# Kernel tuning notes

Hardware: AMD Instinct MI355X
Metric: run time of the kernel (lower is better)

Reference implementation:

```python
import jax, jax.numpy as jnp
import numpy as np

H = 512   # hidden_size
V = 128   # vec_size / output_size
L = 8192  # sequence length


def _gru_cell(x, h, Wih, Whh, bih, bhh):
    # torch GRU cell: gates ordered (r, z, n)
    gx = x @ Wih.T + bih            # [3H]
    gh = h @ Whh.T + bhh            # [3H]
    xr, xz, xn = jnp.split(gx, 3)
    hr, hz, hn = jnp.split(gh, 3)
    r = jax.nn.sigmoid(xr + hr)
    z = jax.nn.sigmoid(xz + hz)
    n = jnp.tanh(xn + r * hn)
    return (1.0 - z) * n + z * h


def _run_gru2(xs, h0, h1, p0, p1):
    """2-layer GRU over xs [L, in]; returns ((h0_f, h1_f), top-layer outputs [L, H])."""
    def step(carry, x):
        c0, c1 = carry
        c0 = _gru_cell(x, c0, *p0)
        c1 = _gru_cell(c0, c1, *p1)
        return (c0, c1), c1
    return jax.lax.scan(step, (h0, h1), xs)


def setup_inputs() -> dict:
    key = jax.random.key(0)
    ks = jax.random.split(key, 24)
    b = 1.0 / np.sqrt(H)  # torch default uniform init bound
    u = lambda k, shape: jax.random.uniform(k, shape, jnp.float32, -b, b)
    inp = {
        "src": jax.random.normal(ks[0], (L, V), jnp.float32),
        "trg": jax.random.uniform(ks[1], (L, V), jnp.float32),
        # encoder GRU (input V -> hidden H, 2 layers)
        "enc_Wih0": u(ks[2], (3 * H, V)),  "enc_Whh0": u(ks[3], (3 * H, H)),
        "enc_bih0": u(ks[4], (3 * H,)),    "enc_bhh0": u(ks[5], (3 * H,)),
        "enc_Wih1": u(ks[6], (3 * H, H)),  "enc_Whh1": u(ks[7], (3 * H, H)),
        "enc_bih1": u(ks[8], (3 * H,)),    "enc_bhh1": u(ks[9], (3 * H,)),
        # decoder GRU (input V -> hidden H, 2 layers)
        "dec_Wih0": u(ks[10], (3 * H, V)), "dec_Whh0": u(ks[11], (3 * H, H)),
        "dec_bih0": u(ks[12], (3 * H,)),   "dec_bhh0": u(ks[13], (3 * H,)),
        "dec_Wih1": u(ks[14], (3 * H, H)), "dec_Whh1": u(ks[15], (3 * H, H)),
        "dec_bih1": u(ks[16], (3 * H,)),   "dec_bhh1": u(ks[17], (3 * H,)),
        # output projection
        "Wout": u(ks[18], (V, H)), "bout": u(ks[19], (V,)),
    }
    return inp


def reference(src, trg,
              enc_Wih0, enc_Whh0, enc_bih0, enc_bhh0,
              enc_Wih1, enc_Whh1, enc_bih1, enc_bhh1,
              dec_Wih0, dec_Whh0, dec_bih0, dec_bhh0,
              dec_Wih1, dec_Whh1, dec_bih1, dec_bhh1,
              Wout, bout):
    z = jnp.zeros((H,), src.dtype)
    # Encoder: run 2-layer GRU over src, keep final per-layer states
    (h0, h1), _ = _run_gru2(
        src, z, z,
        (enc_Wih0, enc_Whh0, enc_bih0, enc_bhh0),
        (enc_Wih1, enc_Whh1, enc_bih1, enc_bhh1))
    # Decoder inputs under full teacher forcing: trg[0], trg[0], trg[1], ... trg[L-2]
    dec_in = jax.nn.relu(jnp.concatenate([trg[:1], trg[:-1]], axis=0))  # [L, V]
    _, ys = _run_gru2(
        dec_in, h0, h1,
        (dec_Wih0, dec_Whh0, dec_bih0, dec_bhh0),
        (dec_Wih1, dec_Whh1, dec_bih1, dec_bhh1))  # ys: [L, H] top-layer outputs
    outputs = jax.nn.sigmoid(ys @ Wout.T + bout)   # [L, V]
    return outputs
```

## Files before the change

kernel.cpp:

```cpp
#include <hip/hip_runtime.h>

#define Hh   512
#define Vv   128
#define LL   8192
#define G3   1536
#define NBK  256
#define NPAIR 1024

#define OFF_GX   0ull
#define OFF_YS   50331648ull
#define OFF_RECE 67108864ull
#define OFF_RECD (OFF_RECE + 16384ull)
#define OFF_WT   (OFF_RECD + 16384ull)

__device__ __forceinline__ float sigm(float x)  { return 1.f / (1.f + __expf(-x)); }
__device__ __forceinline__ float tanha(float x) { return 2.f / (1.f + __expf(-2.f * x)) - 1.f; }

__device__ __forceinline__ unsigned long long packpair(float v, int t) {
    return ((unsigned long long)(unsigned)t << 32) | (unsigned long long)__float_as_uint(v);
}
__device__ __forceinline__ int   pair_tag(unsigned long long p) { return (int)(p >> 32); }
__device__ __forceinline__ float pair_val(unsigned long long p) { return __uint_as_float((unsigned)p); }

__global__ __launch_bounds__(256) void gemm_gx(
    const float* __restrict__ X, const float* __restrict__ Wih,
    const float* __restrict__ bih, float* __restrict__ gxo, int shift_relu)
{
    __shared__ float xs[16][128];
    const int tid = threadIdx.x;
    const int m0  = blockIdx.x * 16;
    const int c   = blockIdx.y * 256 + tid;

    for (int i = tid; i < 16 * 128; i += 256) {
        const int r = i >> 7, k = i & 127;
        int srow = m0 + r;
        if (shift_relu) srow = (srow == 0) ? 0 : (srow - 1);
        float v = X[(size_t)srow * Vv + k];
        if (shift_relu) v = fmaxf(v, 0.f);
        xs[r][k] = v;
    }
    __syncthreads();

    const float4* wp = (const float4*)(Wih + (size_t)c * Vv);
    float4 wr[32];
#pragma unroll
    for (int q = 0; q < 32; ++q) wr[q] = wp[q];
    const float bb = bih[c];

    for (int m = 0; m < 16; ++m) {
        const float4* xp = (const float4*)xs[m];
        float acc = bb;
#pragma unroll
        for (int q = 0; q < 32; ++q) {
            const float4 x4 = xp[q];
            acc = fmaf(wr[q].x, x4.x, acc); acc = fmaf(wr[q].y, x4.y, acc);
            acc = fmaf(wr[q].z, x4.z, acc); acc = fmaf(wr[q].w, x4.w, acc);
        }
        gxo[(size_t)(m0 + m) * G3 + c] = acc;
    }
}

__global__ __launch_bounds__(64, 1) void seq2(
    const float* __restrict__ gx,
    const float* __restrict__ Whh0, const float* __restrict__ Wih1,
    const float* __restrict__ Whh1,
    const float* __restrict__ bhh0, const float* __restrict__ bih1,
    const float* __restrict__ bhh1,
    unsigned long long* __restrict__ rec,
    float* __restrict__ ys)
{
    const int bid  = blockIdx.x, lane = threadIdx.x;
    const int e0   = 2 * bid;

    int off[8];
#pragma unroll
    for (int j = 0; j < 8; ++j) off[j] = (e0 + lane + 64 * j) & 511;

    float w[18][8];
#pragma unroll
    for (int m = 0; m < 3; ++m) {
        const float* mat = (m == 0) ? Whh0 : (m == 1) ? Wih1 : Whh1;
#pragma unroll
        for (int g = 0; g < 3; ++g)
#pragma unroll
            for (int i = 0; i < 2; ++i) {
                const float* row = mat + (size_t)(g * Hh + e0 + i) * Hh;
#pragma unroll
                for (int j = 0; j < 8; ++j) w[m * 6 + g * 2 + i][j] = row[off[j]];
            }
    }

    float b_r = 0.f, b_z = 0.f, b_n1 = 0.f, b_n2 = 0.f;
    if (lane < 2) {
        const int e = e0 + lane;
        b_r = bhh0[e]; b_z = bhh0[Hh + e]; b_n1 = bhh0[2 * Hh + e];
    } else if (lane < 4) {
        const int e = e0 + (lane & 1);
        b_r  = bih1[e] + bhh1[e];
        b_z  = bih1[Hh + e] + bhh1[Hh + e];
        b_n1 = bih1[2 * Hh + e];
        b_n2 = bhh1[2 * Hh + e];
    }

    for (int tau = 0; tau <= LL; ++tau) {
        float xr = 0.f, xz = 0.f, xn = 0.f;
        if (lane < 2 && tau < LL) {
            const size_t gb = (size_t)tau * G3 + e0 + lane;
            xr = gx[gb]; xz = gx[gb + Hh]; xn = gx[gb + 2 * Hh];
        }

        const int need = tau - 1;
        const unsigned long long* rp = rec + (size_t)((tau - 1) & 1) * NPAIR;
        unsigned long long p0[8], p1[8];
        int ok;
        do {
#pragma unroll
            for (int j = 0; j < 8; ++j)
                p0[j] = __hip_atomic_load(rp + off[j],      __ATOMIC_RELAXED, __HIP_MEMORY_SCOPE_AGENT);
#pragma unroll
            for (int j = 0; j < 8; ++j)
                p1[j] = __hip_atomic_load(rp + Hh + off[j], __ATOMIC_RELAXED, __HIP_MEMORY_SCOPE_AGENT);
            ok = 1;
#pragma unroll
            for (int j = 0; j < 8; ++j)
                ok &= (pair_tag(p0[j]) >= need) & (pair_tag(p1[j]) >= need);
        } while (!__all(ok));

        float h0v[8], h1v[8];
#pragma unroll
        for (int j = 0; j < 8; ++j) { h0v[j] = pair_val(p0[j]); h1v[j] = pair_val(p1[j]); }

        float acc[18];
#pragma unroll
        for (int r = 0; r < 18; ++r) acc[r] = 0.f;
#pragma unroll
        for (int j = 0; j < 8; ++j) {
#pragma unroll
            for (int r = 0; r < 12; ++r) acc[r] = fmaf(w[r][j], h0v[j], acc[r]);
#pragma unroll
            for (int r = 12; r < 18; ++r) acc[r] = fmaf(w[r][j], h1v[j], acc[r]);
        }

        float sred[9];
#pragma unroll
        for (int k = 0; k < 9; ++k) {
            float a = acc[2 * k], c = acc[2 * k + 1];
            a += __shfl_xor(a, 1);
            c += __shfl_xor(c, 1);
            float m = (lane & 1) ? c : a;
            m += __shfl_xor(m, 2);  m += __shfl_xor(m, 4);
            m += __shfl_xor(m, 8);  m += __shfl_xor(m, 16);
            m += __shfl_xor(m, 32);
            sred[k] = m;
        }

        const float h1p = __shfl(h1v[0], lane & 1);

        unsigned long long* recw = rec + (size_t)(tau & 1) * NPAIR;
        if (lane < 2) {
            if (tau < LL) {
                const float rg = sigm(xr + sred[0] + b_r);
                const float zg = sigm(xz + sred[1] + b_z);
                const float ng = tanha(xn + rg * (sred[2] + b_n1));
                const float hnew = (1.f - zg) * ng + zg * h0v[0];
                __hip_atomic_store(recw + e0 + lane, packpair(hnew, tau),
                                   __ATOMIC_RELAXED, __HIP_MEMORY_SCOPE_AGENT);
            }
        } else if (lane < 4) {
            const int e = e0 + (lane & 1);
            float hnew;
            if (tau >= 1) {
                const float rg = sigm(sred[3] + sred[6] + b_r);
                const float zg = sigm(sred[4] + sred[7] + b_z);
                const float ng = tanha(sred[5] + b_n1 + rg * (sred[8] + b_n2));
                hnew = (1.f - zg) * ng + zg * h1p;
                if (ys) ys[(size_t)(tau - 1) * Hh + e] = hnew;
            } else {
                hnew = h1p;
            }
            __hip_atomic_store(recw + Hh + e, packpair(hnew, tau),
                               __ATOMIC_RELAXED, __HIP_MEMORY_SCOPE_AGENT);
        }
    }
}

__global__ __launch_bounds__(256) void transposeW(const float* __restrict__ W,
                                                  float* __restrict__ WT,
                                                  unsigned long long* __restrict__ encr)
{
    const int i = blockIdx.x * 256 + threadIdx.x;
    WT[(i & 511) * 128 + (i >> 9)] = W[i];
    if (i < NPAIR) {
        __hip_atomic_store(encr + NPAIR + i, packpair(0.f, -1),
                           __ATOMIC_RELAXED, __HIP_MEMORY_SCOPE_AGENT);
        __hip_atomic_store(encr + i, packpair(0.f, -2),
                           __ATOMIC_RELAXED, __HIP_MEMORY_SCOPE_AGENT);
    }
}

__global__ __launch_bounds__(256) void handoff(const unsigned long long* __restrict__ encr,
                                               unsigned long long* __restrict__ decr)
{
    const int p = blockIdx.x * 256 + threadIdx.x;
    const unsigned long long src = __hip_atomic_load(
        encr + (p < Hh ? NPAIR : 0) + p, __ATOMIC_RELAXED, __HIP_MEMORY_SCOPE_AGENT);
    __hip_atomic_store(decr + NPAIR + p, packpair(pair_val(src), -1),
                       __ATOMIC_RELAXED, __HIP_MEMORY_SCOPE_AGENT);
    __hip_atomic_store(decr + p, packpair(0.f, -2),
                       __ATOMIC_RELAXED, __HIP_MEMORY_SCOPE_AGENT);
}

__global__ __launch_bounds__(128) void out_proj(
    const float* __restrict__ ys, const float* __restrict__ WT,
    const float* __restrict__ bout, float* __restrict__ out)
{
    __shared__ float yss[16][512];
    const int tid = threadIdx.x;
    const int m0  = blockIdx.x * 16;

    for (int i = tid; i < 16 * 512; i += 128)
        yss[i >> 9][i & 511] = ys[(size_t)(m0 + (i >> 9)) * 512 + (i & 511)];
    __syncthreads();

    const int c = tid;
    float acc[16];
    const float b = bout[c];
#pragma unroll
    for (int m = 0; m < 16; ++m) acc[m] = b;

    for (int k4 = 0; k4 < 128; ++k4) {
        const float w0 = WT[(4 * k4 + 0) * 128 + c];
        const float w1 = WT[(4 * k4 + 1) * 128 + c];
        const float w2 = WT[(4 * k4 + 2) * 128 + c];
        const float w3 = WT[(4 * k4 + 3) * 128 + c];
#pragma unroll
        for (int m = 0; m < 16; ++m) {
            const float4 yv = *(const float4*)&yss[m][4 * k4];
            acc[m] = fmaf(w0, yv.x, fmaf(w1, yv.y, fmaf(w2, yv.z, fmaf(w3, yv.w, acc[m]))));
        }
    }
#pragma unroll
    for (int m = 0; m < 16; ++m)
        out[(size_t)(m0 + m) * 128 + c] = 1.f / (1.f + __expf(-acc[m]));
}

extern "C" void kernel_launch(void* const* d_in, const int* in_sizes, int n_in,
                              void* d_out, int out_size, void* d_ws, size_t ws_size,
                              hipStream_t stream)
{
    const float* src      = (const float*)d_in[0];
    const float* trg      = (const float*)d_in[1];
    const float* eWih0    = (const float*)d_in[2];
    const float* eWhh0    = (const float*)d_in[3];
    const float* ebih0    = (const float*)d_in[4];
    const float* ebhh0    = (const float*)d_in[5];
    const float* eWih1    = (const float*)d_in[6];
    const float* eWhh1    = (const float*)d_in[7];
    const float* ebih1    = (const float*)d_in[8];
    const float* ebhh1    = (const float*)d_in[9];
    const float* dWih0    = (const float*)d_in[10];
    const float* dWhh0    = (const float*)d_in[11];
    const float* dbih0    = (const float*)d_in[12];
    const float* dbhh0    = (const float*)d_in[13];
    const float* dWih1    = (const float*)d_in[14];
    const float* dWhh1    = (const float*)d_in[15];
    const float* dbih1    = (const float*)d_in[16];
    const float* dbhh1    = (const float*)d_in[17];
    const float* Wout     = (const float*)d_in[18];
    const float* bout     = (const float*)d_in[19];

    char* ws = (char*)d_ws;
    float*              gx   = (float*)(ws + OFF_GX);
    float*              ys   = (float*)(ws + OFF_YS);
    unsigned long long* recE = (unsigned long long*)(ws + OFF_RECE);
    unsigned long long* recD = (unsigned long long*)(ws + OFF_RECD);
    float*              WT   = (float*)(ws + OFF_WT);

    hipLaunchKernelGGL(transposeW, dim3(256), dim3(256), 0, stream, Wout, WT, recE);

    hipLaunchKernelGGL(gemm_gx, dim3(LL / 16, 6), dim3(256), 0, stream,
                       src, eWih0, ebih0, gx, 0);
    hipLaunchKernelGGL(seq2, dim3(NBK), dim3(64), 0, stream,
                       gx, eWhh0, eWih1, eWhh1, ebhh0, ebih1, ebhh1,
                       recE, (float*)nullptr);

    hipLaunchKernelGGL(handoff, dim3(4), dim3(256), 0, stream, recE, recD);
    hipLaunchKernelGGL(gemm_gx, dim3(LL / 16, 6), dim3(256), 0, stream,
                       trg, dWih0, dbih0, gx, 1);
    hipLaunchKernelGGL(seq2, dim3(NBK), dim3(64), 0, stream,
                       gx, dWhh0, dWih1, dWhh1, dbhh0, dbih1, dbhh1,
                       recD, ys);

    hipLaunchKernelGGL(out_proj, dim3(LL / 16), dim3(128), 0, stream,
                       ys, WT, bout, (float*)d_out);

    (void)in_sizes; (void)n_in; (void)out_size; (void)ws_size;
}
```

Baseline: 37.32 ms.

## Pack four waves per block and share polled hidden state through LDS

The persistent recurrent kernel now runs 64 blocks of 256 threads instead of 256 single-wave blocks. Only wave 0 of each block polls the global tagged-pair exchange buffer, copies the full hidden state into shared memory and publishes a workgroup-scope flag. The other three waves spin on that flag and read the state from LDS. This cuts global polling traffic fourfold, at the cost of an extra intra-block handoff hop on the serial critical path. An empty asm barrier pins the weights in registers.

```diff
diff --git a/kernel.cpp b/kernel.cpp
--- a/kernel.cpp
+++ b/kernel.cpp
@@ -4,7 +4,7 @@
 #define Vv   128
 #define LL   8192
 #define G3   1536
-#define NBK  256
+#define NBLK 64
 #define NPAIR 1024
 
 #define OFF_GX   0ull
@@ -60,7 +60,7 @@
     }
 }
 
-__global__ __launch_bounds__(64, 1) void seq2(
+__global__ __launch_bounds__(256, 1) void seq2(
     const float* __restrict__ gx,
     const float* __restrict__ Whh0, const float* __restrict__ Wih1,
     const float* __restrict__ Whh1,
@@ -69,14 +69,24 @@
     unsigned long long* __restrict__ rec,
     float* __restrict__ ys)
 {
-    const int bid  = blockIdx.x, lane = threadIdx.x;
-    const int e0   = 2 * bid;
+    const int tid  = threadIdx.x;
+    const int lane = tid & 63;
+    const int w    = tid >> 6;
+    const int vb   = blockIdx.x * 4 + w;
+    const int e0   = 2 * vb;
+
+    __shared__ float hbuf[2][1024];
+    __shared__ int   sflag;
+
+    if (tid == 0)
+        __hip_atomic_store(&sflag, -1000000, __ATOMIC_RELAXED, __HIP_MEMORY_SCOPE_WORKGROUP);
+    __syncthreads();
 
     int off[8];
 #pragma unroll
     for (int j = 0; j < 8; ++j) off[j] = (e0 + lane + 64 * j) & 511;
 
-    float w[18][8];
+    float wv[18][8];
 #pragma unroll
     for (int m = 0; m < 3; ++m) {
         const float* mat = (m == 0) ? Whh0 : (m == 1) ? Wih1 : Whh1;
@@ -86,9 +96,14 @@
             for (int i = 0; i < 2; ++i) {
                 const float* row = mat + (size_t)(g * Hh + e0 + i) * Hh;
 #pragma unroll
-                for (int j = 0; j < 8; ++j) w[m * 6 + g * 2 + i][j] = row[off[j]];
+                for (int j = 0; j < 8; ++j) wv[m * 6 + g * 2 + i][j] = row[off[j]];
             }
     }
+#pragma unroll
+    for (int r = 0; r < 18; ++r)
+#pragma unroll
+        for (int j = 0; j < 8; ++j)
+            asm volatile("" : "+v"(wv[r][j]));
 
     float b_r = 0.f, b_z = 0.f, b_n1 = 0.f, b_n2 = 0.f;
     if (lane < 2) {
@@ -110,25 +125,36 @@
         }
 
         const int need = tau - 1;
-        const unsigned long long* rp = rec + (size_t)((tau - 1) & 1) * NPAIR;
-        unsigned long long p0[8], p1[8];
-        int ok;
-        do {
-#pragma unroll
-            for (int j = 0; j < 8; ++j)
-                p0[j] = __hip_atomic_load(rp + off[j],      __ATOMIC_RELAXED, __HIP_MEMORY_SCOPE_AGENT);
-#pragma unroll
-            for (int j = 0; j < 8; ++j)
-                p1[j] = __hip_atomic_load(rp + Hh + off[j], __ATOMIC_RELAXED, __HIP_MEMORY_SCOPE_AGENT);
-            ok = 1;
-#pragma unroll
-            for (int j = 0; j < 8; ++j)
-                ok &= (pair_tag(p0[j]) >= need) & (pair_tag(p1[j]) >= need);
-        } while (!__all(ok));
+        const int s    = need & 1;
+
+        if (w == 0) {
+            const unsigned long long* rp = rec + (size_t)s * NPAIR + lane;
+            unsigned long long p[16];
+            int ok;
+            do {
+#pragma unroll
+                for (int j = 0; j < 16; ++j)
+                    p[j] = __hip_atomic_load(rp + 64 * j, __ATOMIC_RELAXED,
+                                             __HIP_MEMORY_SCOPE_AGENT);
+                ok = 1;
+#pragma unroll
+                for (int j = 0; j < 16; ++j) ok &= (pair_tag(p[j]) >= need);
+            } while (!__all(ok));
+#pragma unroll
+            for (int j = 0; j < 16; ++j)
+                hbuf[s][lane + 64 * j] = pair_val(p[j]);
+            __hip_atomic_store(&sflag, need, __ATOMIC_RELEASE, __HIP_MEMORY_SCOPE_WORKGROUP);
+        } else {
+            while (__hip_atomic_load(&sflag, __ATOMIC_ACQUIRE,
+                                     __HIP_MEMORY_SCOPE_WORKGROUP) < need) {}
+        }
 
         float h0v[8], h1v[8];
 #pragma unroll
-        for (int j = 0; j < 8; ++j) { h0v[j] = pair_val(p0[j]); h1v[j] = pair_val(p1[j]); }
+        for (int j = 0; j < 8; ++j) {
+            h0v[j] = hbuf[s][off[j]];
+            h1v[j] = hbuf[s][512 + off[j]];
+        }
 
         float acc[18];
 #pragma unroll
@@ -136,9 +162,9 @@
 #pragma unroll
         for (int j = 0; j < 8; ++j) {
 #pragma unroll
-            for (int r = 0; r < 12; ++r) acc[r] = fmaf(w[r][j], h0v[j], acc[r]);
-#pragma unroll
-            for (int r = 12; r < 18; ++r) acc[r] = fmaf(w[r][j], h1v[j], acc[r]);
+            for (int r = 0; r < 12; ++r) acc[r] = fmaf(wv[r][j], h0v[j], acc[r]);
+#pragma unroll
+            for (int r = 12; r < 18; ++r) acc[r] = fmaf(wv[r][j], h1v[j], acc[r]);
         }
 
         float sred[9];
@@ -280,14 +306,14 @@
 
     hipLaunchKernelGGL(gemm_gx, dim3(LL / 16, 6), dim3(256), 0, stream,
                        src, eWih0, ebih0, gx, 0);
-    hipLaunchKernelGGL(seq2, dim3(NBK), dim3(64), 0, stream,
+    hipLaunchKernelGGL(seq2, dim3(NBLK), dim3(256), 0, stream,
                        gx, eWhh0, eWih1, eWhh1, ebhh0, ebih1, ebhh1,
                        recE, (float*)nullptr);
 
     hipLaunchKernelGGL(handoff, dim3(4), dim3(256), 0, stream, recE, recD);
     hipLaunchKernelGGL(gemm_gx, dim3(LL / 16, 6), dim3(256), 0, stream,
                        trg, dWih0, dbih0, gx, 1);
-    hipLaunchKernelGGL(seq2, dim3(NBK), dim3(64), 0, stream,
+    hipLaunchKernelGGL(seq2, dim3(NBLK), dim3(256), 0, stream,
                        gx, dWhh0, dWih1, dWhh1, dbhh0, dbih1, dbhh1,
                        recD, ys);
 
```

Measured after the change: 53.87 ms. 44.3% more time.
